# Kernel tuning notes

Hardware: AMD Instinct MI355X
Metric: run time of the kernel (lower is better)

The kernel has to match this reference:

```python
import jax, jax.numpy as jnp
import numpy as np

DIM = 256
HEADS = 4
WIN = 128
PAD = (WIN - 1) // 2  # 63
SHIFT = WIN // 2      # 64
RED = 16              # SE reduction


def _hann(w):
    # torch.hann_window(w, periodic=False)
    n = jnp.arange(w, dtype=jnp.float32)
    return 0.5 * (1.0 - jnp.cos(2.0 * jnp.pi * n / (w - 1)))


def _layernorm(x, g, b, eps=1e-5):
    mu = jnp.mean(x, axis=-1, keepdims=True)
    var = jnp.var(x, axis=-1, keepdims=True)
    return (x - mu) * jax.lax.rsqrt(var + eps) * g + b


def _attend_windows(x, ln_g, ln_b, in_proj_w, in_proj_b, out_w, out_b):
    B, T, C = x.shape
    w = WIN
    h = HEADS
    d = C // h
    L = T + 2 * PAD - w + 1  # number of stride-1 windows (= T-1 for even w)
    y = _layernorm(x, ln_g, ln_b)
    y_pad = jnp.pad(y, ((0, 0), (PAD, PAD), (0, 0)))
    idx = jnp.arange(L)[:, None] + jnp.arange(w)[None, :]  # (L, w)
    win = y_pad[:, idx, :]  # (B, L, w, C) -- the unfold blowup
    win = win * _hann(w)[None, None, :, None]
    # fused qkv projection (torch MHA in_proj)
    qkv = jnp.einsum('blwc,ec->blwe', win, in_proj_w) + in_proj_b  # (B,L,w,3C)
    q, k, v = jnp.split(qkv, 3, axis=-1)
    q = q.reshape(B, L, w, h, d)
    k = k.reshape(B, L, w, h, d)
    v = v.reshape(B, L, w, h, d)
    scale = 1.0 / jnp.sqrt(jnp.asarray(d, dtype=x.dtype))
    scores = jnp.einsum('blqhd,blkhd->blhqk', q, k) * scale
    attn = jax.nn.softmax(scores, axis=-1)
    o = jnp.einsum('blhqk,blkhd->blqhd', attn, v).reshape(B, L, w, C)
    o = jnp.einsum('blwc,ec->blwe', o, out_w) + out_b  # out_proj
    # fold: overlap-add back to length T (crop padding)
    idx_flat = idx.reshape(-1)  # (L*w,)
    acc = jnp.zeros((B, T + 2 * PAD, C), dtype=x.dtype)
    acc = acc.at[:, idx_flat, :].add(o.reshape(B, L * w, C))
    y_out = acc[:, PAD:PAD + T, :]
    counts = jnp.zeros((T + 2 * PAD,), dtype=x.dtype).at[idx_flat].add(1.0)
    counts = counts[PAD:PAD + T]
    return y_out / (counts[None, :, None] + 1e-6)


def setup_inputs() -> dict:
    key = jax.random.key(0)
    ks = jax.random.split(key, 9)
    C = DIM
    s = 0.02
    return {
        'x': jax.random.normal(ks[0], (1, 1024, C), dtype=jnp.float32),
        'ln_g': jnp.ones((C,), jnp.float32),
        'ln_b': jnp.zeros((C,), jnp.float32),
        'in_proj_w': jax.random.normal(ks[1], (3 * C, C), jnp.float32) * s,
        'in_proj_b': jnp.zeros((3 * C,), jnp.float32),
        'out_w': jax.random.normal(ks[2], (C, C), jnp.float32) * s,
        'out_b': jnp.zeros((C,), jnp.float32),
        'proj_w': jax.random.normal(ks[3], (C, C), jnp.float32) * s,
        'proj_b': jnp.zeros((C,), jnp.float32),
        'se_w1': jax.random.normal(ks[4], (C // RED, C), jnp.float32) * s,
        'se_w2': jax.random.normal(ks[5], (C, C // RED), jnp.float32) * s,
    }


def reference(x, ln_g, ln_b, in_proj_w, in_proj_b, out_w, out_b, proj_w, proj_b, se_w1, se_w2):
    # T > window_size branch (1024 > 128)
    y_main = _attend_windows(x, ln_g, ln_b, in_proj_w, in_proj_b, out_w, out_b)
    x_shift = jnp.roll(x, SHIFT, axis=1)
    y_shift = _attend_windows(x_shift, ln_g, ln_b, in_proj_w, in_proj_b, out_w, out_b)
    y_shift = jnp.roll(y_shift, -SHIFT, axis=1)
    y = 0.5 * (y_main + y_shift)
    y = jnp.einsum('btc,ec->bte', y, proj_w) + proj_b  # proj (dropout p=0 -> identity)
    # SE module: global average over T, bottleneck MLP, sigmoid gate
    s = jnp.mean(y, axis=1)  # (B, C)
    s = jax.nn.relu(s @ se_w1.T)
    s = jax.nn.sigmoid(s @ se_w2.T)
    y = y * s[:, None, :]
    return x + y
```

## Files before the change

### kernel.cpp

```cpp
#include <hip/hip_runtime.h>

#define TLEN 1024
#define CDIM 256
#define NHEAD 4
#define HD 64
#define WIN_ 128
#define PADL 63
#define LWIN 1023
#define TPAD 1150
#define SW 32

typedef __attribute__((ext_vector_type(8))) short bf16x8;
typedef __attribute__((ext_vector_type(4))) float f32x4;

__device__ __forceinline__ int prow(int v, int t) {
  if (v == 0) return t;
  if (t < PADL || t >= PADL + TLEN) return t;
  int s = t - PADL;
  s = (s + (TLEN - 64)) & (TLEN - 1);
  return PADL + s;
}

__device__ __forceinline__ float hannf(int j) {
  return 0.5f * (1.0f - __cosf(6.283185307179586f * (float)j / 127.0f));
}

__device__ __forceinline__ float countf(int t) {
  int lo = t - 127; if (lo < 0) lo = 0;
  int hi = t;       if (hi > LWIN - 1) hi = LWIN - 1;
  return (float)(hi - lo + 1);
}

__device__ __forceinline__ unsigned short bfr(float f) {
  unsigned int u = __float_as_uint(f);
  u += 0x7FFFu + ((u >> 16) & 1u);
  return (unsigned short)(u >> 16);
}
__device__ __forceinline__ unsigned int pk2t(float a, float b) {
  return __builtin_amdgcn_perm(__float_as_uint(b), __float_as_uint(a), 0x07060302u);
}
__device__ __forceinline__ float bfu(unsigned short u) {
  return __uint_as_float(((unsigned int)u) << 16);
}
__device__ __forceinline__ float bflo(unsigned int u) { return __uint_as_float(u << 16); }
__device__ __forceinline__ float bfhi(unsigned int u) { return __uint_as_float(u & 0xFFFF0000u); }

#define AL16(h, l) ((((unsigned int)(l)) >> 16) | (((unsigned int)(h)) << 16))

__global__ void k_prep(const float* __restrict__ x, const float* __restrict__ g,
                       const float* __restrict__ b, unsigned short* __restrict__ lnbf,
                       const float* __restrict__ W, unsigned short* __restrict__ Wb,
                       const float* __restrict__ pw, const float* __restrict__ ow,
                       const float* __restrict__ ob, unsigned short* __restrict__ Mtb,
                       float* __restrict__ vbv,
                       float* __restrict__ accg, unsigned short* __restrict__ Pbf,
                       float* __restrict__ msum) {
  __shared__ float pr[256];
  __shared__ float red[256];
  const int bid = blockIdx.x;
  const int tid = threadIdx.x;
  if (bid < 256) {
    int wv = tid >> 6, lane = tid & 63;
    int r = bid * 4 + wv;
    float4 v = ((const float4*)(x + (size_t)r * CDIM))[lane];
    float s = v.x + v.y + v.z + v.w;
    float q = v.x * v.x + v.y * v.y + v.z * v.z + v.w * v.w;
    #pragma unroll
    for (int m = 32; m >= 1; m >>= 1) { s += __shfl_xor(s, m); q += __shfl_xor(q, m); }
    float mu = s * (1.0f / 256.0f);
    float var = q * (1.0f / 256.0f) - mu * mu;
    float rs = rsqrtf(var + 1e-5f);
    float4 gg = ((const float4*)g)[lane];
    float4 bb = ((const float4*)b)[lane];
    uint2 o;
    o.x = (unsigned int)bfr((v.x - mu) * rs * gg.x + bb.x) |
          ((unsigned int)bfr((v.y - mu) * rs * gg.y + bb.y) << 16);
    o.y = (unsigned int)bfr((v.z - mu) * rs * gg.z + bb.z) |
          ((unsigned int)bfr((v.w - mu) * rs * gg.w + bb.w) << 16);
    ((uint2*)(lnbf + (size_t)r * CDIM))[lane] = o;
  } else if (bid < 352) {
    int i = (bid - 256) * 256 + tid;
    const float4* src = (const float4*)W;
    float4 a = src[2 * i], c = src[2 * i + 1];
    uint4 o;
    o.x = (unsigned int)bfr(a.x) | ((unsigned int)bfr(a.y) << 16);
    o.y = (unsigned int)bfr(a.z) | ((unsigned int)bfr(a.w) << 16);
    o.z = (unsigned int)bfr(c.x) | ((unsigned int)bfr(c.y) << 16);
    o.w = (unsigned int)bfr(c.z) | ((unsigned int)bfr(c.w) << 16);
    ((uint4*)Wb)[i] = o;
  } else if (bid < 608) {
    const int e = bid - 352;
    pr[tid] = pw[(size_t)e * CDIM + tid];
    __syncthreads();
    float a0 = 0.f, a1 = 0.f, a2 = 0.f, a3 = 0.f;
    for (int m = 0; m < 256; m += 4) {
      a0 += pr[m] * ow[(size_t)m * CDIM + tid];
      a1 += pr[m + 1] * ow[(size_t)(m + 1) * CDIM + tid];
      a2 += pr[m + 2] * ow[(size_t)(m + 2) * CDIM + tid];
      a3 += pr[m + 3] * ow[(size_t)(m + 3) * CDIM + tid];
    }
    Mtb[(size_t)e * CDIM + tid] = bfr((a0 + a1) + (a2 + a3));
    red[tid] = pr[tid] * ob[tid];
    __syncthreads();
    for (int s = 128; s > 0; s >>= 1) { if (tid < s) red[tid] += red[tid + s]; __syncthreads(); }
    if (tid == 0) vbv[e] = red[0];
  } else if (bid < 624) {
    uint4 zz = make_uint4(0, 0, 0, 0);
    for (int i = (bid - 608) * 256 + tid; i < 147200; i += 16 * 256)
      ((uint4*)accg)[i] = zz;
  } else {
    uint4 zz = make_uint4(0, 0, 0, 0);
    for (int i = (bid - 624) * 256 + tid; i < 12096; i += 16 * 256) {
      int idx = (i < 6048) ? i : (104352 + (i - 6048));
      ((uint4*)Pbf)[idx] = zz;
    }
    if (bid == 624 && tid < 64) ((float4*)msum)[tid] = make_float4(0.f, 0.f, 0.f, 0.f);
  }
}

__launch_bounds__(512, 1)
__global__ void k_proj(const unsigned short* __restrict__ lnbf,
                       const unsigned short* __restrict__ Wb,
                       unsigned short* __restrict__ Pbf) {
  __shared__ __align__(16) unsigned short Ps[64 * 128];
  const int tid = threadIdx.x;
  const int lane = tid & 63, wv = tid >> 6;
  const int li16 = lane & 15, q4 = lane >> 4;
  const int ws = wv & 1, we = wv >> 1;
  const int sbase = blockIdx.x * 64;
  const int ebase = blockIdx.y * 128;
  const int s0 = sbase + ws * 32;
  const int e0 = ebase + we * 32;

  f32x4 acc[2][2];
  #pragma unroll
  for (int it = 0; it < 2; ++it)
    #pragma unroll
    for (int et = 0; et < 2; ++et) acc[it][et] = (f32x4){0.f, 0.f, 0.f, 0.f};

  #pragma unroll
  for (int ks = 0; ks < 8; ++ks) {
    bf16x8 Af[2], Bf[2];
    #pragma unroll
    for (int it = 0; it < 2; ++it)
      Af[it] = *(const bf16x8*)(lnbf + (size_t)(s0 + 16 * it + li16) * 256 + ks * 32 + q4 * 8);
    #pragma unroll
    for (int et = 0; et < 2; ++et)
      Bf[et] = *(const bf16x8*)(Wb + (size_t)(e0 + 16 * et + li16) * 256 + ks * 32 + q4 * 8);
    #pragma unroll
    for (int it = 0; it < 2; ++it)
      #pragma unroll
      for (int et = 0; et < 2; ++et)
        acc[it][et] = __builtin_amdgcn_mfma_f32_16x16x32_bf16(Af[it], Bf[et], acc[it][et], 0, 0, 0);
  }
  #pragma unroll
  for (int it = 0; it < 2; ++it)
    #pragma unroll
    for (int et = 0; et < 2; ++et)
      #pragma unroll
      for (int r = 0; r < 4; ++r) {
        int lr = ws * 32 + 16 * it + 4 * q4 + r;
        int lc = we * 32 + 16 * et + li16;
        Ps[lr * 128 + lc] = bfr(acc[it][et][r]);
      }
  __syncthreads();
  for (int i = tid; i < 1024; i += 512) {
    int r = i >> 4, c = (i & 15) * 8;
    *(uint4*)(Pbf + (size_t)(PADL + sbase + r) * 768 + ebase + c) = *(uint4*)&Ps[r * 128 + c];
  }
}

__device__ __forceinline__ void stage_v(const unsigned short* __restrict__ Pbf,
                                        unsigned short* vt, int v, int hd,
                                        int l0, int w, int tid,
                                        const float* __restrict__ bB,
                                        const float* __restrict__ hth) {
  const int jp = tid & 63;
  const int dg = tid >> 6;
  const int j0 = 2 * jp;
  const int p0 = w + j0;
  int row0 = prow(v, l0 + w + j0);
  int row1 = prow(v, l0 + w + j0 + 1);
  uint4 a = *(const uint4*)(Pbf + (size_t)row0 * 768 + 512 + hd * 64 + dg * 8);
  uint4 b = *(const uint4*)(Pbf + (size_t)row1 * 768 + 512 + hd * 64 + dg * 8);
  float h0 = hth[j0], h1 = hth[j0 + 1];
  float e0 = __expf(h0 * bB[p0] * 0.125f);
  float e1 = __expf(h1 * bB[p0 + 1] * 0.125f);
  float f0 = e0 * h0, f1 = e1 * h1;
  unsigned int av[4] = {a.x, a.y, a.z, a.w};
  unsigned int bv[4] = {b.x, b.y, b.z, b.w};
  #pragma unroll
  for (int q = 0; q < 4; ++q) {
    int d0 = dg * 8 + 2 * q;
    unsigned int w0 = pk2t(f0 * bflo(av[q]), f1 * bflo(bv[q]));
    unsigned int w1 = pk2t(f0 * bfhi(av[q]), f1 * bfhi(bv[q]));
    *(unsigned int*)&vt[d0 * 128 + (j0 ^ ((d0 & 7) << 3))] = w0;
    *(unsigned int*)&vt[(d0 + 1) * 128 + (j0 ^ (((d0 + 1) & 7) << 3))] = w1;
  }
  if (tid < 64) {
    *(unsigned int*)&vt[64 * 128 + j0] = pk2t(e0, e1);
  }
}

__launch_bounds__(512, 2)
__global__ void k_attn(const unsigned short* __restrict__ Pbf, const float* __restrict__ ipb,
                       float* __restrict__ accg) {
  __shared__ __align__(16) unsigned short band[160 * 168];
  __shared__ __align__(16) unsigned short Vt[2][80 * 128];
  __shared__ __align__(16) unsigned char uni[159 * 68 * 4];
  __shared__ float hth[128];
  __shared__ float bB[160];
  __shared__ float bqS[64];

  unsigned short* Pq = (unsigned short*)uni;
  unsigned short* Pk = Pq + 159 * 64;
  float* accs = (float*)uni;

  const int strip = blockIdx.x, hd = blockIdx.y, v = blockIdx.z;
  const int l0 = strip * SW;
  const int nw = (SW < LWIN - l0) ? SW : (LWIN - l0);
  const int span = nw - 1 + WIN_;
  const int tid = threadIdx.x;
  const int lane = tid & 63, wv = tid >> 6;
  const int li16 = lane & 15, q4 = lane >> 4;
  const int iw = 16 * wv + li16;

  if (tid < 128) hth[tid] = hannf(tid);
  if (tid < 64) bqS[tid] = ipb[hd * 64 + tid];
  for (int i = tid; i < span * 8; i += 512) {
    int t = i >> 3, dg = i & 7;
    int row = prow(v, l0 + t);
    const unsigned short* src = Pbf + (size_t)row * 768 + hd * 64;
    uint4 q = *(const uint4*)(src + dg * 8);
    uint4 k = *(const uint4*)(src + 256 + dg * 8);
    int off = (dg * 8) ^ ((t & 7) << 3);
    *(uint4*)&Pq[t * 64 + off] = q;
    *(uint4*)&Pk[t * 64 + off] = k;
  }
  {
    uint4 zz = make_uint4(0, 0, 0, 0);
    for (int i = tid; i < 480; i += 512) {
      int bidx = i / 240, k = i % 240;
      *(uint4*)&Vt[bidx][65 * 128 + k * 8] = zz;
    }
  }
  __syncthreads();

  for (int p = tid; p < span; p += 512) {
    float b = 0.0f;
    int sw = (p & 7) << 3;
    for (int d = 0; d < 64; ++d) b += bqS[d] * bfu(Pk[p * 64 + (d ^ sw)]);
    bB[p] = b;
  }
  for (int tile = wv; tile < 100; tile += 8) {
    int ta = tile / 10, tb = tile - 10 * (tile / 10);
    int tqa = 16 * ta + li16, swq = (tqa & 7) << 3;
    bf16x8 Aq0 = *(bf16x8*)&Pq[tqa * 64 + ((8 * q4) ^ swq)];
    bf16x8 Aq1 = *(bf16x8*)&Pq[tqa * 64 + ((32 + 8 * q4) ^ swq)];
    int tkb = 16 * tb + li16, swk = (tkb & 7) << 3;
    bf16x8 Bk0 = *(bf16x8*)&Pk[tkb * 64 + ((8 * q4) ^ swk)];
    bf16x8 Bk1 = *(bf16x8*)&Pk[tkb * 64 + ((32 + 8 * q4) ^ swk)];
    f32x4 D = (f32x4){0.f, 0.f, 0.f, 0.f};
    D = __builtin_amdgcn_mfma_f32_16x16x32_bf16(Aq0, Bk0, D, 0, 0, 0);
    D = __builtin_amdgcn_mfma_f32_16x16x32_bf16(Aq1, Bk1, D, 0, 0, 0);
    #pragma unroll
    for (int r = 0; r < 4; ++r)
      band[(16 * ta + 4 * q4 + r) * 168 + 16 * tb + li16] = bfr(D[r]);
  }
  __syncthreads();

  for (int i = tid; i < 159 * 68; i += 512) accs[i] = 0.0f;
  stage_v(Pbf, &Vt[0][0], v, hd, l0, 0, tid, bB, hth);
  __syncthreads();

  float hh2[32];
  {
    const float h_i = hth[iw];
    #pragma unroll
    for (int ks = 0; ks < 4; ++ks)
      #pragma unroll
      for (int jj = 0; jj < 8; ++jj)
        hh2[ks * 8 + jj] = h_i * hth[32 * ks + 8 * q4 + jj] * 0.125f;
  }

  #pragma unroll 1
  for (int w = 0; w < nw; ++w) {
    const int m = w & 7;
    const unsigned short* brow = &band[(w + iw) * 168 + (w & ~7)];
    const unsigned short* vt = &Vt[w & 1][0];

    f32x4 O[5];
    #pragma unroll
    for (int mt = 0; mt < 5; ++mt) O[mt] = (f32x4){0.f, 0.f, 0.f, 0.f};

    #pragma unroll
    for (int ks = 0; ks < 4; ++ks) {
      uint4 R0 = *(const uint4*)&brow[32 * ks + 8 * q4];
      uint4 R1 = *(const uint4*)&brow[32 * ks + 8 * q4 + 8];
      unsigned int d0 = R0.x, d1 = R0.y, d2 = R0.z, d3 = R0.w;
      unsigned int d4 = R1.x, d5 = R1.y, d6 = R1.z, d7 = R1.w;
      unsigned int o0, o1, o2, o3;
      switch (m) {
        case 0: o0 = d0; o1 = d1; o2 = d2; o3 = d3; break;
        case 1: o0 = AL16(d1, d0); o1 = AL16(d2, d1); o2 = AL16(d3, d2); o3 = AL16(d4, d3); break;
        case 2: o0 = d1; o1 = d2; o2 = d3; o3 = d4; break;
        case 3: o0 = AL16(d2, d1); o1 = AL16(d3, d2); o2 = AL16(d4, d3); o3 = AL16(d5, d4); break;
        case 4: o0 = d2; o1 = d3; o2 = d4; o3 = d5; break;
        case 5: o0 = AL16(d3, d2); o1 = AL16(d4, d3); o2 = AL16(d5, d4); o3 = AL16(d6, d5); break;
        case 6: o0 = d3; o1 = d4; o2 = d5; o3 = d6; break;
        default: o0 = AL16(d4, d3); o1 = AL16(d5, d4); o2 = AL16(d6, d5); o3 = AL16(d7, d6); break;
      }
      float a0 = __expf(hh2[ks * 8 + 0] * bflo(o0));
      float a1 = __expf(hh2[ks * 8 + 1] * bfhi(o0));
      float a2 = __expf(hh2[ks * 8 + 2] * bflo(o1));
      float a3 = __expf(hh2[ks * 8 + 3] * bfhi(o1));
      float a4 = __expf(hh2[ks * 8 + 4] * bflo(o2));
      float a5 = __expf(hh2[ks * 8 + 5] * bfhi(o2));
      float a6 = __expf(hh2[ks * 8 + 6] * bflo(o3));
      float a7 = __expf(hh2[ks * 8 + 7] * bfhi(o3));
      union { uint4 u; bf16x8 f; } cvt;
      cvt.u.x = pk2t(a0, a1);
      cvt.u.y = pk2t(a2, a3);
      cvt.u.z = pk2t(a4, a5);
      cvt.u.w = pk2t(a6, a7);
      bf16x8 Bf = cvt.f;

      #pragma unroll
      for (int mt = 0; mt < 5; ++mt) {
        int d = 16 * mt + li16;
        bf16x8 Af = *(bf16x8*)&vt[d * 128 + ((32 * ks + 8 * q4) ^ ((d & 7) << 3))];
        O[mt] = __builtin_amdgcn_mfma_f32_16x16x32_bf16(Af, Bf, O[mt], 0, 0, 0);
      }
    }

    float nn = __shfl(O[4][0], li16);
    float sc = 1.0f / nn;

    {
      float* arow = &accs[(w + iw) * 68];
      #pragma unroll
      for (int mt = 0; mt < 4; ++mt) {
        int c = 16 * mt + 4 * q4;
        float4 cur = *(float4*)&arow[c];
        cur.x += O[mt][0] * sc; cur.y += O[mt][1] * sc;
        cur.z += O[mt][2] * sc; cur.w += O[mt][3] * sc;
        *(float4*)&arow[c] = cur;
      }
    }

    if (w + 1 < nw) stage_v(Pbf, &Vt[(w + 1) & 1][0], v, hd, l0, w + 1, tid, bB, hth);
    __syncthreads();
  }

  float* av = accg + (size_t)v * TPAD * CDIM;
  for (int i = tid; i < span * 64; i += 512) {
    int p = i >> 6, dd = i & 63;
    int lo = p - 127; if (lo < 0) lo = 0;
    int hi = p; if (hi > nw - 1) hi = nw - 1;
    float cnt = (float)(hi - lo + 1);
    float bvd = ipb[512 + hd * 64 + dd];
    atomicAdd(&av[(size_t)(l0 + p) * CDIM + hd * 64 + dd],
              accs[p * 68 + dd] + cnt * bvd);
  }
}

__launch_bounds__(512, 2)
__global__ void k_comb(const float* __restrict__ accg, const unsigned short* __restrict__ Mtb,
                       const float* __restrict__ vbv, const float* __restrict__ pb,
                       float* __restrict__ z, float* __restrict__ msum) {
  __shared__ __align__(16) unsigned short Ub[32 * 264];
  __shared__ float cfA[32], cfB[32], bscL[32];
  __shared__ float msB[128];
  const int tid = threadIdx.x;
  const int lane = tid & 63, wv = tid >> 6;
  const int li16 = lane & 15, q4 = lane >> 4;
  const int t0 = blockIdx.x * 32;
  const int e0 = blockIdx.y * 128;

  if (tid < 32) {
    int s = t0 + tid;
    float c0 = countf(PADL + s);
    float c1 = countf(PADL + ((s + 64) & (TLEN - 1)));
    float fA = 0.5f / (c0 + 1e-6f), fB = 0.5f / (c1 + 1e-6f);
    cfA[tid] = fA; cfB[tid] = fB;
    bscL[tid] = c0 * fA + c1 * fB;
  }
  if (tid < 128) msB[tid] = 0.0f;
  __syncthreads();

  for (int i = tid; i < 32 * 128; i += 512) {
    int rr = i >> 7, c2 = (i & 127) * 2;
    int s = t0 + rr;
    int s1 = (s + 64) & (TLEN - 1);
    float2 a0 = *(const float2*)&accg[(size_t)(PADL + s) * CDIM + c2];
    float2 a1 = *(const float2*)&accg[(size_t)TPAD * CDIM + (size_t)(PADL + s1) * CDIM + c2];
    float fA = cfA[rr], fB = cfB[rr];
    *(unsigned int*)&Ub[rr * 264 + c2] =
        pk2t(a0.x * fA + a1.x * fB, a0.y * fA + a1.y * fB);
  }
  __syncthreads();

  f32x4 acc[2];
  acc[0] = (f32x4){0.f, 0.f, 0.f, 0.f};
  acc[1] = (f32x4){0.f, 0.f, 0.f, 0.f};
  #pragma unroll
  for (int ks = 0; ks < 8; ++ks) {
    bf16x8 Bf = *(const bf16x8*)(Mtb + (size_t)(e0 + wv * 16 + li16) * 256 + ks * 32 + q4 * 8);
    #pragma unroll
    for (int it = 0; it < 2; ++it) {
      bf16x8 Af = *(bf16x8*)&Ub[(16 * it + li16) * 264 + ks * 32 + q4 * 8];
      acc[it] = __builtin_amdgcn_mfma_f32_16x16x32_bf16(Af, Bf, acc[it], 0, 0, 0);
    }
  }

  {
    int e = e0 + wv * 16 + li16;
    float vbe = vbv[e], pbe = pb[e];
    float part = 0.0f;
    #pragma unroll
    for (int it = 0; it < 2; ++it)
      #pragma unroll
      for (int r = 0; r < 4; ++r) {
        int rloc = 16 * it + 4 * q4 + r;
        float val = acc[it][r] + bscL[rloc] * vbe + pbe;
        z[(size_t)(t0 + rloc) * CDIM + e] = val;
        part += val;
      }
    atomicAdd(&msB[e - e0], part);
  }
  __syncthreads();
  if (tid < 128) atomicAdd(&msum[e0 + tid], msB[tid]);
}

__global__ void k_finalse(const float* __restrict__ x, const float* __restrict__ z,
                          const float* __restrict__ msum, const float* __restrict__ w1,
                          const float* __restrict__ w2, float* __restrict__ out) {
  __shared__ float red2[16][4];
  __shared__ float s1[16];
  __shared__ float gateS[256];
  int tid = threadIdx.x;
  int lane = tid & 63, wv = tid >> 6;
  float sm = msum[tid] * (1.0f / 1024.0f);
  #pragma unroll
  for (int r = 0; r < 16; ++r) {
    float v = sm * w1[(size_t)r * 256 + tid];
    #pragma unroll
    for (int m = 32; m >= 1; m >>= 1) v += __shfl_xor(v, m);
    if (lane == 0) red2[r][wv] = v;
  }
  __syncthreads();
  if (tid < 16) {
    float a = red2[tid][0] + red2[tid][1] + red2[tid][2] + red2[tid][3];
    s1[tid] = fmaxf(a, 0.0f);
  }
  __syncthreads();
  float gacc = 0.0f;
  #pragma unroll
  for (int i = 0; i < 16; ++i) gacc += s1[i] * w2[(size_t)tid * 16 + i];
  gateS[tid] = 1.0f / (1.0f + __expf(-gacc));
  __syncthreads();
  int i = blockIdx.x * 256 + tid;
  float4 xv = ((const float4*)x)[i];
  float4 zv = ((const float4*)z)[i];
  float4 gv = ((const float4*)gateS)[i & 63];
  float4 o;
  o.x = xv.x + zv.x * gv.x;
  o.y = xv.y + zv.y * gv.y;
  o.z = xv.z + zv.z * gv.z;
  o.w = xv.w + zv.w * gv.w;
  ((float4*)out)[i] = o;
}

extern "C" void kernel_launch(void* const* d_in, const int* in_sizes, int n_in,
                              void* d_out, int out_size, void* d_ws, size_t ws_size,
                              hipStream_t stream) {
  const float* x   = (const float*)d_in[0];
  const float* lng = (const float*)d_in[1];
  const float* lnb = (const float*)d_in[2];
  const float* ipw = (const float*)d_in[3];
  const float* ipb = (const float*)d_in[4];
  const float* ow  = (const float*)d_in[5];
  const float* ob  = (const float*)d_in[6];
  const float* pw  = (const float*)d_in[7];
  const float* pb  = (const float*)d_in[8];
  const float* w1  = (const float*)d_in[9];
  const float* w2  = (const float*)d_in[10];
  float* out = (float*)d_out;

  float* ws = (float*)d_ws;
  unsigned short* lnbf = (unsigned short*)ws;
  unsigned short* Wb   = (unsigned short*)(ws + 131072);
  unsigned short* Pbf  = (unsigned short*)(ws + 229376);
  float* accg = ws + 229376 + 441600;
  unsigned short* Mtb = (unsigned short*)(accg + 588800);
  float* vbv  = accg + 588800 + 32768;
  float* z    = vbv + 256;
  float* msum = z + 262144;

  k_prep<<<dim3(640), dim3(256), 0, stream>>>(x, lng, lnb, lnbf, ipw, Wb,
                                              pw, ow, ob, Mtb, vbv, accg, Pbf, msum);
  k_proj<<<dim3(16, 6), dim3(512), 0, stream>>>(lnbf, Wb, Pbf);
  k_attn<<<dim3(32, NHEAD, 2), dim3(512), 0, stream>>>(Pbf, ipb, accg);
  k_comb<<<dim3(32, 2), dim3(512), 0, stream>>>(accg, Mtb, vbv, pb, z, msum);
  k_finalse<<<dim3(256), dim3(256), 0, stream>>>(x, z, msum, w1, w2, out);
}
```

Measured before the change: 185.3 us.

## Prefetch next V tile into registers, use raw exp2, and raise MFMA priority

Splits V staging into a global load and an LDS write. The load for window w+1 is issued at the top of iteration w, so its latency overlaps the exp and MFMA work. It replaces __expf with the hardware v_exp_f32 and folds the 0.125*log2(e) factor into the precomputed hann and bias terms, saving a multiply per exponential. The MFMA section is wrapped in s_setprio, and the per-window LDS accumulation becomes per-element LDS atomicAdd, which adds LDS instructions for no apparent correctness need.

```diff
diff --git a/kernel.cpp b/kernel.cpp
--- a/kernel.cpp
+++ b/kernel.cpp
@@ -45,7 +45,15 @@
 __device__ __forceinline__ float bflo(unsigned int u) { return __uint_as_float(u << 16); }
 __device__ __forceinline__ float bfhi(unsigned int u) { return __uint_as_float(u & 0xFFFF0000u); }
 
+__device__ __forceinline__ float ex2(float x) {
+  float r;
+  asm("v_exp_f32 %0, %1" : "=v"(r) : "v"(x));
+  return r;
+}
+
 #define AL16(h, l) ((((unsigned int)(l)) >> 16) | (((unsigned int)(h)) << 16))
+
+#define QLOG2E 0.18033688011112042f
 
 __global__ void k_prep(const float* __restrict__ x, const float* __restrict__ g,
                        const float* __restrict__ b, unsigned short* __restrict__ lnbf,
@@ -170,22 +178,29 @@
   }
 }
 
-__device__ __forceinline__ void stage_v(const unsigned short* __restrict__ Pbf,
-                                        unsigned short* vt, int v, int hd,
-                                        int l0, int w, int tid,
-                                        const float* __restrict__ bB,
-                                        const float* __restrict__ hth) {
+__device__ __forceinline__ void stage_load(const unsigned short* __restrict__ Pbf,
+                                           int v, int hd, int l0, int w, int tid,
+                                           uint4& A, uint4& B) {
+  const int jp = tid & 63;
+  const int dg = tid >> 6;
+  const int j0 = 2 * jp;
+  int row0 = prow(v, l0 + w + j0);
+  int row1 = prow(v, l0 + w + j0 + 1);
+  A = *(const uint4*)(Pbf + (size_t)row0 * 768 + 512 + hd * 64 + dg * 8);
+  B = *(const uint4*)(Pbf + (size_t)row1 * 768 + 512 + hd * 64 + dg * 8);
+}
+
+__device__ __forceinline__ void stage_write(unsigned short* vt, int w, int tid,
+                                            const float* __restrict__ bB,
+                                            const float* __restrict__ hth,
+                                            uint4 a, uint4 b) {
   const int jp = tid & 63;
   const int dg = tid >> 6;
   const int j0 = 2 * jp;
   const int p0 = w + j0;
-  int row0 = prow(v, l0 + w + j0);
-  int row1 = prow(v, l0 + w + j0 + 1);
-  uint4 a = *(const uint4*)(Pbf + (size_t)row0 * 768 + 512 + hd * 64 + dg * 8);
-  uint4 b = *(const uint4*)(Pbf + (size_t)row1 * 768 + 512 + hd * 64 + dg * 8);
   float h0 = hth[j0], h1 = hth[j0 + 1];
-  float e0 = __expf(h0 * bB[p0] * 0.125f);
-  float e1 = __expf(h1 * bB[p0 + 1] * 0.125f);
+  float e0 = ex2(h0 * bB[p0]);
+  float e1 = ex2(h1 * bB[p0 + 1]);
   float f0 = e0 * h0, f1 = e1 * h1;
   unsigned int av[4] = {a.x, a.y, a.z, a.w};
   unsigned int bv[4] = {b.x, b.y, b.z, b.w};
@@ -224,6 +239,9 @@
   const int lane = tid & 63, wv = tid >> 6;
   const int li16 = lane & 15, q4 = lane >> 4;
   const int iw = 16 * wv + li16;
+
+  uint4 sA, sB;
+  stage_load(Pbf, v, hd, l0, 0, tid, sA, sB);
 
   if (tid < 128) hth[tid] = hannf(tid);
   if (tid < 64) bqS[tid] = ipb[hd * 64 + tid];
@@ -250,7 +268,7 @@
     float b = 0.0f;
     int sw = (p & 7) << 3;
     for (int d = 0; d < 64; ++d) b += bqS[d] * bfu(Pk[p * 64 + (d ^ sw)]);
-    bB[p] = b;
+    bB[p] = b * QLOG2E;
   }
   for (int tile = wv; tile < 100; tile += 8) {
     int ta = tile / 10, tb = tile - 10 * (tile / 10);
@@ -270,7 +288,7 @@
   __syncthreads();
 
   for (int i = tid; i < 159 * 68; i += 512) accs[i] = 0.0f;
-  stage_v(Pbf, &Vt[0][0], v, hd, l0, 0, tid, bB, hth);
+  stage_write(&Vt[0][0], 0, tid, bB, hth, sA, sB);
   __syncthreads();
 
   float hh2[32];
@@ -280,11 +298,13 @@
     for (int ks = 0; ks < 4; ++ks)
       #pragma unroll
       for (int jj = 0; jj < 8; ++jj)
-        hh2[ks * 8 + jj] = h_i * hth[32 * ks + 8 * q4 + jj] * 0.125f;
+        hh2[ks * 8 + jj] = h_i * hth[32 * ks + 8 * q4 + jj] * QLOG2E;
   }
 
   #pragma unroll 1
   for (int w = 0; w < nw; ++w) {
+    if (w + 1 < nw) stage_load(Pbf, v, hd, l0, w + 1, tid, sA, sB);
+
     const int m = w & 7;
     const unsigned short* brow = &band[(w + iw) * 168 + (w & ~7)];
     const unsigned short* vt = &Vt[w & 1][0];
@@ -293,6 +313,7 @@
     #pragma unroll
     for (int mt = 0; mt < 5; ++mt) O[mt] = (f32x4){0.f, 0.f, 0.f, 0.f};
 
+    __builtin_amdgcn_s_setprio(1);
     #pragma unroll
     for (int ks = 0; ks < 4; ++ks) {
       uint4 R0 = *(const uint4*)&brow[32 * ks + 8 * q4];
@@ -310,14 +331,14 @@
         case 6: o0 = d3; o1 = d4; o2 = d5; o3 = d6; break;
         default: o0 = AL16(d4, d3); o1 = AL16(d5, d4); o2 = AL16(d6, d5); o3 = AL16(d7, d6); break;
       }
-      float a0 = __expf(hh2[ks * 8 + 0] * bflo(o0));
-      float a1 = __expf(hh2[ks * 8 + 1] * bfhi(o0));
-      float a2 = __expf(hh2[ks * 8 + 2] * bflo(o1));
-      float a3 = __expf(hh2[ks * 8 + 3] * bfhi(o1));
-      float a4 = __expf(hh2[ks * 8 + 4] * bflo(o2));
-      float a5 = __expf(hh2[ks * 8 + 5] * bfhi(o2));
-      float a6 = __expf(hh2[ks * 8 + 6] * bflo(o3));
-      float a7 = __expf(hh2[ks * 8 + 7] * bfhi(o3));
+      float a0 = ex2(hh2[ks * 8 + 0] * bflo(o0));
+      float a1 = ex2(hh2[ks * 8 + 1] * bfhi(o0));
+      float a2 = ex2(hh2[ks * 8 + 2] * bflo(o1));
+      float a3 = ex2(hh2[ks * 8 + 3] * bfhi(o1));
+      float a4 = ex2(hh2[ks * 8 + 4] * bflo(o2));
+      float a5 = ex2(hh2[ks * 8 + 5] * bfhi(o2));
+      float a6 = ex2(hh2[ks * 8 + 6] * bflo(o3));
+      float a7 = ex2(hh2[ks * 8 + 7] * bfhi(o3));
       union { uint4 u; bf16x8 f; } cvt;
       cvt.u.x = pk2t(a0, a1);
       cvt.u.y = pk2t(a2, a3);
@@ -332,6 +353,7 @@
         O[mt] = __builtin_amdgcn_mfma_f32_16x16x32_bf16(Af, Bf, O[mt], 0, 0, 0);
       }
     }
+    __builtin_amdgcn_s_setprio(0);
 
     float nn = __shfl(O[4][0], li16);
     float sc = 1.0f / nn;
@@ -341,14 +363,14 @@
       #pragma unroll
       for (int mt = 0; mt < 4; ++mt) {
         int c = 16 * mt + 4 * q4;
-        float4 cur = *(float4*)&arow[c];
-        cur.x += O[mt][0] * sc; cur.y += O[mt][1] * sc;
-        cur.z += O[mt][2] * sc; cur.w += O[mt][3] * sc;
-        *(float4*)&arow[c] = cur;
+        atomicAdd(&arow[c + 0], O[mt][0] * sc);
+        atomicAdd(&arow[c + 1], O[mt][1] * sc);
+        atomicAdd(&arow[c + 2], O[mt][2] * sc);
+        atomicAdd(&arow[c + 3], O[mt][3] * sc);
       }
     }
 
-    if (w + 1 < nw) stage_v(Pbf, &Vt[(w + 1) & 1][0], v, hd, l0, w + 1, tid, bB, hth);
+    if (w + 1 < nw) stage_write(&Vt[(w + 1) & 1][0], w + 1, tid, bB, hth, sA, sB);
     __syncthreads();
   }
 
```

Result: slower. 500.1 us (+169.8%).
